# Performance work log

Hardware: AMD Instinct MI355X
Metric: run time of the kernel (lower is better)

The kernel has to match this reference:

```python
import jax, jax.numpy as jnp
import numpy as np
from jax import lax

N, P, Z, L = 1000, 50000, 10, 5


def setup_inputs() -> dict:
    key = jax.random.key(0)
    ks = jax.random.split(key, 9)
    data = jax.random.normal(ks[0], (N, P), dtype=jnp.float32)
    mean_z = jax.random.normal(ks[1], (N, Z), dtype=jnp.float32)
    A = jax.random.normal(ks[2], (Z, Z), dtype=jnp.float32) * 0.1
    var_z = A @ A.T + 0.01 * jnp.eye(Z, dtype=jnp.float32)  # PSD
    mean_w = jax.random.normal(ks[3], (L, Z, P), dtype=jnp.float32) * 0.01
    var_w = jax.random.uniform(ks[4], (L, Z), dtype=jnp.float32) + 0.1   # positive
    alpha = jax.nn.softmax(jax.random.normal(ks[5], (L, Z, P), dtype=jnp.float32), axis=-1)
    tau_0 = jax.random.uniform(ks[6], (L, Z), dtype=jnp.float32) + 0.5   # positive prior precision
    pi = jax.nn.softmax(jax.random.normal(ks[7], (Z, P), dtype=jnp.float32), axis=-1)
    tau = jnp.array(1.0, dtype=jnp.float32)
    return dict(data=data, mean_z=mean_z, var_z=var_z, mean_w=mean_w,
                var_w=var_w, alpha=alpha, tau_0=tau_0, pi=pi, tau=tau)


def _log_bf(z, s2, s0):
    s0_inv = 1.0 / s0
    s2ps0inv = s2 + s0_inv
    return 0.5 * (jnp.log(s2) - jnp.log(s2ps0inv) + z ** 2 * (s0_inv / s2ps0inv))


def reference(data, mean_z, var_z, mean_w, var_w, alpha, tau_0, pi, tau):
    n_dim = data.shape[0]
    l_dim, z_dim, p_dim = mean_w.shape

    # FactorModel.moments
    mean_zz = mean_z.T @ mean_z + n_dim * var_z            # [z, z]
    # LoadingModel.moments (only mean_w moment is needed)
    W0 = jnp.sum(mean_w * alpha, axis=0)                    # [z, p]

    def factor_body(kdx, carry):
        W, mw, vw, al = carry
        not_k = jnp.where(jnp.arange(z_dim) != kdx, size=z_dim - 1)[0]  # [z-1]
        E_zpzk = mean_zz[kdx][not_k]                        # [z-1]
        E_zzk = mean_zz[kdx, kdx]                           # scalar
        Wk = W[kdx]                                         # [p]
        Wnk = W[not_k]                                      # [z-1, p]
        RtZk = mean_z[:, kdx] @ data - Wnk.T @ E_zpzk       # [p]

        def effect_body(ldx, ecarry):
            Wk, mw, vw, al = ecarry
            Wkl = Wk - mw[ldx, kdx] * al[ldx, kdx]          # [p] residualized
            E_RtZk = RtZk - E_zzk * Wkl                     # [p]
            u_var = jnp.reciprocal(tau * E_zzk + tau_0[ldx, kdx])  # scalar
            u_mean = tau * u_var * E_RtZk                   # [p]
            Z_s = E_RtZk / E_zzk * jnp.sqrt(E_zzk * tau)    # [p]
            s2_s = 1.0 / (E_zzk * tau)
            log_bf = _log_bf(Z_s, s2_s, tau_0[ldx, kdx])
            alpha_kl = jax.nn.softmax(jnp.log(pi[kdx]) + log_bf)   # [p]
            Wk_new = Wkl + u_mean * alpha_kl
            return (Wk_new,
                    mw.at[ldx, kdx].set(u_mean),
                    vw.at[ldx, kdx].set(u_var),
                    al.at[ldx, kdx].set(alpha_kl))

        Wk, mw, vw, al = lax.fori_loop(0, l_dim, effect_body, (Wk, mw, vw, al))
        return (W.at[kdx].set(Wk), mw, vw, al)

    W, mw, vw, al = lax.fori_loop(0, z_dim, factor_body, (W0, mean_w, var_w, alpha))
    return mw, vw, al
```

## Files before the change

kernel.cpp:

```cpp
#include <hip/hip_runtime.h>
#include <math.h>

#define N_DIM 1000
#define P_DIM 50000
#define Z_DIM 10
#define L_DIM 5
#define NSTEP 50

#define NTP 256
#define NBP 196
#define NSPLIT 4
#define NCHUNK 250

#define NT1 1024
#define NBLK 49
#define NEG_BIG (-3.0e38f)
#define SPIN_MAX 32768

constexpr size_t ZP       = (size_t)Z_DIM * P_DIM;
constexpr size_t OFF_ZTR  = 0;
constexpr size_t OFF_PART = ZP;
constexpr size_t PART_F   = (size_t)NSTEP * 64 * 2;
constexpr size_t OFF_ZZ   = ZP + PART_F;
constexpr size_t WS_ZERO_BYTES = (ZP + PART_F) * sizeof(float);

constexpr size_t OUT_MW = 0;
constexpr size_t OUT_VW = (size_t)L_DIM * Z_DIM * P_DIM;
constexpr size_t OUT_AL = OUT_VW + (size_t)L_DIM * Z_DIM;

__device__ inline void online_merge(float& m, float& e, float m2, float e2) {
    float M = fmaxf(m, m2);
    e = e * __expf(m - M) + e2 * __expf(m2 - M);
    m = M;
}

__global__ __launch_bounds__(256) void init_zz(const float* __restrict__ mean_z,
                                               const float* __restrict__ var_z,
                                               float* __restrict__ ws) {
    float* zz = ws + OFF_ZZ;
    int i = blockIdx.x / Z_DIM, j = blockIdx.x % Z_DIM;
    float s = 0.f;
    for (int n = threadIdx.x; n < N_DIM; n += 256)
        s += mean_z[n * Z_DIM + i] * mean_z[n * Z_DIM + j];
    #pragma unroll
    for (int off = 32; off > 0; off >>= 1) s += __shfl_xor(s, off);
    __shared__ float ls[4];
    if ((threadIdx.x & 63) == 0) ls[threadIdx.x >> 6] = s;
    __syncthreads();
    if (threadIdx.x == 0) {
        float t = ls[0] + ls[1] + ls[2] + ls[3];
        zz[blockIdx.x] = t + (float)N_DIM * var_z[blockIdx.x];
    }
}

__global__ __launch_bounds__(NTP) void precompute_big(const float* __restrict__ data,
                                                      const float* __restrict__ mean_z,
                                                      float* __restrict__ ws) {
    float* ZtR = ws + OFF_ZTR;
    __shared__ float mzs[NCHUNK * Z_DIM];
    int n0 = blockIdx.y * NCHUNK;
    for (int i = threadIdx.x; i < NCHUNK * Z_DIM; i += NTP)
        mzs[i] = mean_z[n0 * Z_DIM + i];
    __syncthreads();
    int p = blockIdx.x * NTP + threadIdx.x;
    if (p >= P_DIM) return;

    float acc[Z_DIM];
    #pragma unroll
    for (int z = 0; z < Z_DIM; z++) acc[z] = 0.f;
    for (int r = 0; r < NCHUNK; r++) {
        float d = data[(size_t)(n0 + r) * P_DIM + p];
        #pragma unroll
        for (int z = 0; z < Z_DIM; z++) acc[z] = fmaf(mzs[r * Z_DIM + z], d, acc[z]);
    }
    #pragma unroll
    for (int z = 0; z < Z_DIM; z++) atomicAdd(&ZtR[(size_t)z * P_DIM + p], acc[z]);
}

__global__ __launch_bounds__(NT1) void steps_coop(const float* __restrict__ mw0,
                                                  const float* __restrict__ al0,
                                                  const float* __restrict__ pi,
                                                  const float* __restrict__ tau0,
                                                  const float* __restrict__ taup,
                                                  float* __restrict__ ws,
                                                  float* __restrict__ out) {
    const float* ZtR = ws + OFF_ZTR;
    const float* zz  = ws + OFF_ZZ;
    unsigned long long* part = reinterpret_cast<unsigned long long*>(ws + OFF_PART);
    float* out_mw = out + OUT_MW;
    float* out_vw = out + OUT_VW;
    float* out_al = out + OUT_AL;

    __shared__ float sm[NT1 / 64], se[NT1 / 64], bro[2];

    const int tid  = threadIdx.x;
    const int bid  = blockIdx.x;
    const int lane = tid & 63;
    const int wid  = tid >> 6;
    const int p    = bid * NT1 + tid;
    const bool valid = p < P_DIM;
    const float tau = taup[0];

    float W[Z_DIM], Zt[Z_DIM];
    #pragma unroll
    for (int z = 0; z < Z_DIM; z++) { W[z] = 0.f; Zt[z] = 0.f; }
    float mw_c = 0.f, al_c = 0.f, lpi = 0.f;
    if (valid) {
        #pragma unroll
        for (int z = 0; z < Z_DIM; z++) Zt[z] = ZtR[(size_t)z * P_DIM + p];
        #pragma unroll
        for (int z = 0; z < Z_DIM; z++) {
            float w = 0.f;
            #pragma unroll
            for (int l = 0; l < L_DIM; l++) {
                size_t io = ((size_t)l * Z_DIM + z) * P_DIM + p;
                w = fmaf(mw0[io], al0[io], w);
            }
            W[z] = w;
        }
        mw_c = mw0[p];
        al_c = al0[p];
        lpi  = __logf(pi[p]);
    }

    float wk = 0.f, r = 0.f;
    int k = 0, l = 0;

    #pragma unroll 1
    for (int s = 0; s < NSTEP; s++) {
        const float Ezz   = zz[k * Z_DIM + k];
        const float t0v   = tau0[l * Z_DIM + k];
        const float u_var = 1.f / (tau * Ezz + t0v);
        const float s2    = 1.f / (Ezz * tau);
        const float s0inv = 1.f / t0v;
        const float cq    = 0.5f * (tau / Ezz) * (s0inv / (s2 + s0inv));

        if (l == 0) {
            float rr = 0.f, wkk = 0.f;
            #pragma unroll
            for (int j = 0; j < Z_DIM; j++) {
                float zkj = zz[k * Z_DIM + j];
                if (j == k) { rr += Zt[j]; wkk = W[j]; }
                else        { rr = fmaf(-zkj, W[j], rr); }
            }
            r = rr; wk = wkk;
        }

        const size_t io = ((size_t)l * Z_DIM + k) * P_DIM + p;
        float wkl = 0.f, um = 0.f, lgt = NEG_BIG;
        float m = NEG_BIG, e = 0.f;
        if (valid) {
            wkl = wk - mw_c * al_c;
            float E = fmaf(-Ezz, wkl, r);
            um  = tau * u_var * E;
            lgt = fmaf(cq * E, E, lpi);
            out_mw[io] = um;
            m = lgt; e = 1.f;
        }

        #pragma unroll
        for (int off = 32; off > 0; off >>= 1)
            online_merge(m, e, __shfl_xor(m, off), __shfl_xor(e, off));
        if (lane == 0) { sm[wid] = m; se[wid] = e; }
        __syncthreads();
        if (tid == 0) {
            float M = sm[0], E = se[0];
            #pragma unroll
            for (int w = 1; w < NT1 / 64; w++) online_merge(M, E, sm[w], se[w]);
            unsigned long long v = ((unsigned long long)__float_as_uint(E) << 32)
                                 | (unsigned long long)__float_as_uint(M);
            __hip_atomic_store(&part[(size_t)s * 64 + bid], v, __ATOMIC_RELAXED,
                               __HIP_MEMORY_SCOPE_AGENT);
        }

        int kn = k, ln = l + 1;
        if (ln == L_DIM) { ln = 0; kn++; }
        float mw_n = 0.f, al_n = 0.f, lpi_n = lpi;
        if (valid && s + 1 < NSTEP) {
            size_t ion = ((size_t)ln * Z_DIM + kn) * P_DIM + p;
            mw_n = mw0[ion];
            al_n = al0[ion];
            if (ln == 0) lpi_n = __logf(pi[(size_t)kn * P_DIM + p]);
        }

        float pm = NEG_BIG, pe = 0.f;
        if (wid == 0) {
            if (lane < NBLK) {
                const unsigned long long* ap = &part[(size_t)s * 64 + lane];
                unsigned long long v = 0;
                for (int it = 0; it < SPIN_MAX; it++) {
                    v = __hip_atomic_load(ap, __ATOMIC_RELAXED, __HIP_MEMORY_SCOPE_AGENT);
                    if ((unsigned)(v >> 32) != 0u) break;
                }
                pm = __uint_as_float((unsigned)v);
                pe = __uint_as_float((unsigned)(v >> 32));
            }
            #pragma unroll
            for (int off = 32; off > 0; off >>= 1)
                online_merge(pm, pe, __shfl_xor(pm, off), __shfl_xor(pe, off));
            if (lane == 0) { bro[0] = pm; bro[1] = pe; }
        }
        __syncthreads();
        const float M    = bro[0];
        const float Sinv = 1.f / bro[1];

        if (valid) {
            float a = __expf(lgt - M) * Sinv;
            out_al[io] = a;
            wk = fmaf(um, a, wkl);
        }
        if (p == 0) out_vw[l * Z_DIM + k] = u_var;

        if (l == L_DIM - 1) {
            #pragma unroll
            for (int j = 0; j < Z_DIM; j++) if (j == k) W[j] = wk;
        }
        mw_c = mw_n; al_c = al_n; lpi = lpi_n;
        k = kn; l = ln;
    }
}

extern "C" void kernel_launch(void* const* d_in, const int* in_sizes, int n_in,
                              void* d_out, int out_size, void* d_ws, size_t ws_size,
                              hipStream_t stream) {
    (void)in_sizes; (void)n_in; (void)out_size; (void)ws_size;
    const float* data   = (const float*)d_in[0];
    const float* mean_z = (const float*)d_in[1];
    const float* var_z  = (const float*)d_in[2];
    const float* mw0    = (const float*)d_in[3];
    const float* al0    = (const float*)d_in[5];
    const float* tau0   = (const float*)d_in[6];
    const float* pi     = (const float*)d_in[7];
    const float* taup   = (const float*)d_in[8];
    float* out = (float*)d_out;
    float* ws  = (float*)d_ws;

    hipMemsetAsync(ws, 0, WS_ZERO_BYTES, stream);
    init_zz<<<Z_DIM * Z_DIM, 256, 0, stream>>>(mean_z, var_z, ws);
    precompute_big<<<dim3(NBP, NSPLIT), NTP, 0, stream>>>(data, mean_z, ws);
    steps_coop<<<NBLK, NT1, 0, stream>>>(mw0, al0, pi, tau0, taup, ws, out);
}
```

Baseline: 531.7 us.

## Process four P elements per thread with 256-thread blocks and precomputed W

The step kernel now uses 256 threads per block, each handling four consecutive p positions with float4 loads and stores. The block softmax reduction becomes a two-pass max-then-sum, which replaces the online merge. The initial W sum over L moves into precompute_big, and ZtR rows are loaded only when needed. This is meant to cut per-step __syncthreads cost across 16 waves, give each thread more independent work and vectorize memory traffic, at the cost of more registers per thread and an extra workspace buffer.

```diff
diff --git a/kernel.cpp b/kernel.cpp
--- a/kernel.cpp
+++ b/kernel.cpp
@@ -12,7 +12,9 @@
 #define NSPLIT 4
 #define NCHUNK 250
 
-#define NT1 1024
+#define NT1 256
+#define PPT 4
+#define PBLK (NT1 * PPT)
 #define NBLK 49
 #define NEG_BIG (-3.0e38f)
 #define SPIN_MAX 32768
@@ -21,7 +23,8 @@
 constexpr size_t OFF_ZTR  = 0;
 constexpr size_t OFF_PART = ZP;
 constexpr size_t PART_F   = (size_t)NSTEP * 64 * 2;
-constexpr size_t OFF_ZZ   = ZP + PART_F;
+constexpr size_t OFF_W    = ZP + PART_F;
+constexpr size_t OFF_ZZ   = OFF_W + ZP;
 constexpr size_t WS_ZERO_BYTES = (ZP + PART_F) * sizeof(float);
 
 constexpr size_t OUT_MW = 0;
@@ -55,8 +58,11 @@
 
 __global__ __launch_bounds__(NTP) void precompute_big(const float* __restrict__ data,
                                                       const float* __restrict__ mean_z,
+                                                      const float* __restrict__ mw0,
+                                                      const float* __restrict__ al0,
                                                       float* __restrict__ ws) {
     float* ZtR = ws + OFF_ZTR;
+    float* W   = ws + OFF_W;
     __shared__ float mzs[NCHUNK * Z_DIM];
     int n0 = blockIdx.y * NCHUNK;
     for (int i = threadIdx.x; i < NCHUNK * Z_DIM; i += NTP)
@@ -75,16 +81,30 @@
     }
     #pragma unroll
     for (int z = 0; z < Z_DIM; z++) atomicAdd(&ZtR[(size_t)z * P_DIM + p], acc[z]);
-}
-
-__global__ __launch_bounds__(NT1) void steps_coop(const float* __restrict__ mw0,
-                                                  const float* __restrict__ al0,
-                                                  const float* __restrict__ pi,
-                                                  const float* __restrict__ tau0,
-                                                  const float* __restrict__ taup,
-                                                  float* __restrict__ ws,
-                                                  float* __restrict__ out) {
+
+    if (blockIdx.y == 0) {
+        #pragma unroll
+        for (int z = 0; z < Z_DIM; z++) {
+            float w = 0.f;
+            #pragma unroll
+            for (int l = 0; l < L_DIM; l++) {
+                size_t io = ((size_t)l * Z_DIM + z) * P_DIM + p;
+                w = fmaf(mw0[io], al0[io], w);
+            }
+            W[(size_t)z * P_DIM + p] = w;
+        }
+    }
+}
+
+__global__ __launch_bounds__(NT1) void steps_fused(const float* __restrict__ mw0,
+                                                   const float* __restrict__ al0,
+                                                   const float* __restrict__ pi,
+                                                   const float* __restrict__ tau0,
+                                                   const float* __restrict__ taup,
+                                                   float* __restrict__ ws,
+                                                   float* __restrict__ out) {
     const float* ZtR = ws + OFF_ZTR;
+    const float* Wg  = ws + OFF_W;
     const float* zz  = ws + OFF_ZZ;
     unsigned long long* part = reinterpret_cast<unsigned long long*>(ws + OFF_PART);
     float* out_mw = out + OUT_MW;
@@ -97,33 +117,37 @@
     const int bid  = blockIdx.x;
     const int lane = tid & 63;
     const int wid  = tid >> 6;
-    const int p    = bid * NT1 + tid;
-    const bool valid = p < P_DIM;
+    const int p0   = bid * PBLK + tid * PPT;
+    const bool valid = p0 < P_DIM;
     const float tau = taup[0];
 
-    float W[Z_DIM], Zt[Z_DIM];
-    #pragma unroll
-    for (int z = 0; z < Z_DIM; z++) { W[z] = 0.f; Zt[z] = 0.f; }
-    float mw_c = 0.f, al_c = 0.f, lpi = 0.f;
+    float W[Z_DIM][PPT];
+    #pragma unroll
+    for (int z = 0; z < Z_DIM; z++)
+        #pragma unroll
+        for (int i = 0; i < PPT; i++) W[z][i] = 0.f;
     if (valid) {
         #pragma unroll
-        for (int z = 0; z < Z_DIM; z++) Zt[z] = ZtR[(size_t)z * P_DIM + p];
-        #pragma unroll
         for (int z = 0; z < Z_DIM; z++) {
-            float w = 0.f;
-            #pragma unroll
-            for (int l = 0; l < L_DIM; l++) {
-                size_t io = ((size_t)l * Z_DIM + z) * P_DIM + p;
-                w = fmaf(mw0[io], al0[io], w);
-            }
-            W[z] = w;
-        }
-        mw_c = mw0[p];
-        al_c = al0[p];
-        lpi  = __logf(pi[p]);
-    }
-
-    float wk = 0.f, r = 0.f;
+            float4 t = *reinterpret_cast<const float4*>(Wg + (size_t)z * P_DIM + p0);
+            W[z][0] = t.x; W[z][1] = t.y; W[z][2] = t.z; W[z][3] = t.w;
+        }
+    }
+    float mw_c[PPT], al_c[PPT], lpi[PPT];
+    #pragma unroll
+    for (int i = 0; i < PPT; i++) { mw_c[i] = 0.f; al_c[i] = 0.f; lpi[i] = 0.f; }
+    if (valid) {
+        float4 tm = *reinterpret_cast<const float4*>(mw0 + p0);
+        float4 ta = *reinterpret_cast<const float4*>(al0 + p0);
+        mw_c[0] = tm.x; mw_c[1] = tm.y; mw_c[2] = tm.z; mw_c[3] = tm.w;
+        al_c[0] = ta.x; al_c[1] = ta.y; al_c[2] = ta.z; al_c[3] = ta.w;
+        #pragma unroll
+        for (int i = 0; i < PPT; i++) lpi[i] = __logf(pi[p0 + i]);
+    }
+
+    float wk[PPT], r[PPT];
+    #pragma unroll
+    for (int i = 0; i < PPT; i++) { wk[i] = 0.f; r[i] = 0.f; }
     int k = 0, l = 0;
 
     #pragma unroll 1
@@ -136,51 +160,77 @@
         const float cq    = 0.5f * (tau / Ezz) * (s0inv / (s2 + s0inv));
 
         if (l == 0) {
-            float rr = 0.f, wkk = 0.f;
+            float zk[PPT] = {0.f, 0.f, 0.f, 0.f};
+            if (valid) {
+                float4 t = *reinterpret_cast<const float4*>(ZtR + (size_t)k * P_DIM + p0);
+                zk[0] = t.x; zk[1] = t.y; zk[2] = t.z; zk[3] = t.w;
+            }
+            #pragma unroll
+            for (int i = 0; i < PPT; i++) r[i] = zk[i];
             #pragma unroll
             for (int j = 0; j < Z_DIM; j++) {
-                float zkj = zz[k * Z_DIM + j];
-                if (j == k) { rr += Zt[j]; wkk = W[j]; }
-                else        { rr = fmaf(-zkj, W[j], rr); }
-            }
-            r = rr; wk = wkk;
-        }
-
-        const size_t io = ((size_t)l * Z_DIM + k) * P_DIM + p;
-        float wkl = 0.f, um = 0.f, lgt = NEG_BIG;
-        float m = NEG_BIG, e = 0.f;
+                float c = (j == k) ? 0.f : zz[k * Z_DIM + j];
+                #pragma unroll
+                for (int i = 0; i < PPT; i++) r[i] = fmaf(-c, W[j][i], r[i]);
+                if (j == k)
+                    #pragma unroll
+                    for (int i = 0; i < PPT; i++) wk[i] = W[j][i];
+            }
+        }
+
+        const size_t io = ((size_t)l * Z_DIM + k) * P_DIM + p0;
+        float wkl[PPT], um[PPT], lgt[PPT];
+        #pragma unroll
+        for (int i = 0; i < PPT; i++) { wkl[i] = 0.f; um[i] = 0.f; lgt[i] = NEG_BIG; }
         if (valid) {
-            wkl = wk - mw_c * al_c;
-            float E = fmaf(-Ezz, wkl, r);
-            um  = tau * u_var * E;
-            lgt = fmaf(cq * E, E, lpi);
-            out_mw[io] = um;
-            m = lgt; e = 1.f;
-        }
-
-        #pragma unroll
-        for (int off = 32; off > 0; off >>= 1)
-            online_merge(m, e, __shfl_xor(m, off), __shfl_xor(e, off));
-        if (lane == 0) { sm[wid] = m; se[wid] = e; }
+            #pragma unroll
+            for (int i = 0; i < PPT; i++) {
+                wkl[i] = wk[i] - mw_c[i] * al_c[i];
+                float E = fmaf(-Ezz, wkl[i], r[i]);
+                um[i]  = tau * u_var * E;
+                lgt[i] = fmaf(cq * E, E, lpi[i]);
+            }
+            float4 sv = make_float4(um[0], um[1], um[2], um[3]);
+            *reinterpret_cast<float4*>(out_mw + io) = sv;
+        }
+
+        float m4 = fmaxf(fmaxf(lgt[0], lgt[1]), fmaxf(lgt[2], lgt[3]));
+        #pragma unroll
+        for (int off = 32; off > 0; off >>= 1) m4 = fmaxf(m4, __shfl_xor(m4, off));
+        if (lane == 0) sm[wid] = m4;
+        __syncthreads();
+        const float Mb = fmaxf(fmaxf(sm[0], sm[1]), fmaxf(sm[2], sm[3]));
+
+        float esv[PPT];
+        #pragma unroll
+        for (int i = 0; i < PPT; i++) esv[i] = __expf(lgt[i] - Mb);
+        float s4 = (esv[0] + esv[1]) + (esv[2] + esv[3]);
+        #pragma unroll
+        for (int off = 32; off > 0; off >>= 1) s4 += __shfl_xor(s4, off);
+        if (lane == 0) se[wid] = s4;
         __syncthreads();
         if (tid == 0) {
-            float M = sm[0], E = se[0];
-            #pragma unroll
-            for (int w = 1; w < NT1 / 64; w++) online_merge(M, E, sm[w], se[w]);
-            unsigned long long v = ((unsigned long long)__float_as_uint(E) << 32)
-                                 | (unsigned long long)__float_as_uint(M);
+            float Eb = (se[0] + se[1]) + (se[2] + se[3]);
+            unsigned long long v = ((unsigned long long)__float_as_uint(Eb) << 32)
+                                 | (unsigned long long)__float_as_uint(Mb);
             __hip_atomic_store(&part[(size_t)s * 64 + bid], v, __ATOMIC_RELAXED,
                                __HIP_MEMORY_SCOPE_AGENT);
         }
 
         int kn = k, ln = l + 1;
         if (ln == L_DIM) { ln = 0; kn++; }
-        float mw_n = 0.f, al_n = 0.f, lpi_n = lpi;
+        float mw_n[PPT], al_n[PPT], lpi_n[PPT];
+        #pragma unroll
+        for (int i = 0; i < PPT; i++) { mw_n[i] = 0.f; al_n[i] = 0.f; lpi_n[i] = lpi[i]; }
         if (valid && s + 1 < NSTEP) {
-            size_t ion = ((size_t)ln * Z_DIM + kn) * P_DIM + p;
-            mw_n = mw0[ion];
-            al_n = al0[ion];
-            if (ln == 0) lpi_n = __logf(pi[(size_t)kn * P_DIM + p]);
+            size_t ion = ((size_t)ln * Z_DIM + kn) * P_DIM + p0;
+            float4 tm = *reinterpret_cast<const float4*>(mw0 + ion);
+            float4 ta = *reinterpret_cast<const float4*>(al0 + ion);
+            mw_n[0] = tm.x; mw_n[1] = tm.y; mw_n[2] = tm.z; mw_n[3] = tm.w;
+            al_n[0] = ta.x; al_n[1] = ta.y; al_n[2] = ta.z; al_n[3] = ta.w;
+            if (ln == 0)
+                #pragma unroll
+                for (int i = 0; i < PPT; i++) lpi_n[i] = __logf(pi[(size_t)kn * P_DIM + p0 + i]);
         }
 
         float pm = NEG_BIG, pe = 0.f;
@@ -201,21 +251,30 @@
             if (lane == 0) { bro[0] = pm; bro[1] = pe; }
         }
         __syncthreads();
-        const float M    = bro[0];
-        const float Sinv = 1.f / bro[1];
+        const float M = bro[0];
+        const float scale = __expf(Mb - M) / bro[1];
 
         if (valid) {
-            float a = __expf(lgt - M) * Sinv;
-            out_al[io] = a;
-            wk = fmaf(um, a, wkl);
-        }
-        if (p == 0) out_vw[l * Z_DIM + k] = u_var;
+            float a[PPT];
+            #pragma unroll
+            for (int i = 0; i < PPT; i++) {
+                a[i] = esv[i] * scale;
+                wk[i] = fmaf(um[i], a[i], wkl[i]);
+            }
+            float4 sv = make_float4(a[0], a[1], a[2], a[3]);
+            *reinterpret_cast<float4*>(out_al + io) = sv;
+        }
+        if (p0 == 0 && tid == 0) out_vw[l * Z_DIM + k] = u_var;
 
         if (l == L_DIM - 1) {
             #pragma unroll
-            for (int j = 0; j < Z_DIM; j++) if (j == k) W[j] = wk;
-        }
-        mw_c = mw_n; al_c = al_n; lpi = lpi_n;
+            for (int j = 0; j < Z_DIM; j++)
+                if (j == k)
+                    #pragma unroll
+                    for (int i = 0; i < PPT; i++) W[j][i] = wk[i];
+        }
+        #pragma unroll
+        for (int i = 0; i < PPT; i++) { mw_c[i] = mw_n[i]; al_c[i] = al_n[i]; lpi[i] = lpi_n[i]; }
         k = kn; l = ln;
     }
 }
@@ -237,6 +296,6 @@
 
     hipMemsetAsync(ws, 0, WS_ZERO_BYTES, stream);
     init_zz<<<Z_DIM * Z_DIM, 256, 0, stream>>>(mean_z, var_z, ws);
-    precompute_big<<<dim3(NBP, NSPLIT), NTP, 0, stream>>>(data, mean_z, ws);
-    steps_coop<<<NBLK, NT1, 0, stream>>>(mw0, al0, pi, tau0, taup, ws, out);
-}
+    precompute_big<<<dim3(NBP, NSPLIT), NTP, 0, stream>>>(data, mean_z, mw0, al0, ws);
+    steps_fused<<<NBLK, NT1, 0, stream>>>(mw0, al0, pi, tau0, taup, ws, out);
+}
```

New measurement: 476.6 us. 10.4% less time.
